# Kernel tuning notes

Measured on AMD Instinct MI355X. Metric: run time of the kernel, lower is better.

## Reference

```python
import jax, jax.numpy as jnp
import numpy as np

B, S, HID = 4, 4096, 1024
HEADS, D = 8, 128          # head_dim = HID // HEADS
NSEG, SEGLEN = 16, 256     # SEGLEN = S // NSEG
E, I = 16, 512             # num_experts, intermediate_size


def setup_inputs() -> dict:
    key = jax.random.key(0)
    ks = jax.random.split(key, 8)
    return {
        "x": jax.random.normal(ks[0], (B, S, HID), jnp.float32),
        "W_mh": jax.random.normal(ks[1], (HID, HID), jnp.float32) * (1.0 / np.sqrt(HID)),
        "b_mh": jax.random.normal(ks[2], (HID,), jnp.float32) * 0.02,
        "W_merge": jax.random.normal(ks[3], (HID, HID), jnp.float32) * (1.0 / np.sqrt(HID)),
        "b_merge": jnp.zeros((HID,), jnp.float32),
        "expert_embeddings": jax.random.normal(ks[4], (D, E), jnp.float32) * (1.0 / np.sqrt(D)),
        "first_linear": jax.random.normal(ks[5], (E, I, D), jnp.float32) * (1.0 / np.sqrt(D)),
        "second_linear": jax.random.normal(ks[6], (E, D, I), jnp.float32) * (1.0 / np.sqrt(I)),
    }


def reference(x, W_mh, b_mh, W_merge, b_merge, expert_embeddings, first_linear, second_linear):
    # multi-head projection
    x = x @ W_mh.T + b_mh                                   # [B,S,HID]
    # split into segments/heads (faithful to torch reshape order)
    x = x.reshape(B, NSEG, SEGLEN, HEADS, D)                # [B,N,L,H,D]
    avg = jnp.mean(x, axis=2)                               # [B,N,H,D]
    # router: softmax over experts
    ew = jax.nn.softmax(jnp.einsum('bnhd,de->bnhe', avg, expert_embeddings), axis=-1)
    # merge expert weight matrices (equivalent to torch's broadcast-mul-sum)
    m1 = jnp.einsum('eid,bnhe->bnhid', first_linear, ew)    # [B,N,H,I,D]
    m2 = jnp.einsum('edi,bnhe->bnhdi', second_linear, ew)   # [B,N,H,D,I]
    # NOTE: torch uses reshape (not permute) here -> mixes seglen/head axes; replicate.
    xr = x.reshape(B, NSEG, HEADS, SEGLEN, D)               # [B,N,H,L,D]
    # causal shift: segment s uses weights from segment s-1
    x_causal = xr[:, 1:]
    h = jax.nn.relu(jnp.einsum('bnhld,bnhid->bnhli', x_causal, m1[:, :-1]))
    res = jnp.einsum('bnhli,bnhdi->bnhld', h, m2[:, :-1])   # [B,N-1,H,L,D]
    # segment 0 special case (no_grad in torch -> stop_gradient)
    h0 = jax.nn.relu(jnp.einsum('bhld,bhid->bhli', xr[:, 0], m1[:, 0]))
    r0 = jnp.einsum('bhli,bhdi->bhld', h0, m2[:, 0])
    r0 = jax.lax.stop_gradient(r0)[:, None]                 # [B,1,H,L,D]
    out = jnp.concatenate([r0, res], axis=1)                # [B,N,H,L,D]
    out = out.reshape(B, S, HEADS, D).reshape(B, S, HID)
    return out @ W_merge.T + b_merge
```

## Files before the change

### kernel.cpp

```cpp
#include <hip/hip_runtime.h>
#include <hip/hip_bf16.h>

typedef _Float16 f16;
typedef f16 f16x2 __attribute__((ext_vector_type(2)));
typedef f16 f16x4 __attribute__((ext_vector_type(4)));
typedef f16 f16x8 __attribute__((ext_vector_type(8)));
typedef float f32x2 __attribute__((ext_vector_type(2)));
typedef float f32x4 __attribute__((ext_vector_type(4)));

#define MFMA16(a, b, c) __builtin_amdgcn_mfma_f32_16x16x32_f16(a, b, c, 0, 0, 0)

__device__ __forceinline__ void glds16(const void* g, void* l) {
    __builtin_amdgcn_global_load_lds(
        (const __attribute__((address_space(1))) unsigned int*)g,
        (__attribute__((address_space(3))) unsigned int*)l, 16, 0, 0);
}

__global__ __launch_bounds__(256) void cvt_kernel(const float* __restrict__ s,
                                                  f16* __restrict__ d, int n) {
    int i = (blockIdx.x * 256 + threadIdx.x) * 8;
    if (i >= n) return;
    float4 a = *(const float4*)(s + i);
    float4 b = *(const float4*)(s + i + 4);
    f16x8 h;
    h[0] = (f16)a.x; h[1] = (f16)a.y; h[2] = (f16)a.z; h[3] = (f16)a.w;
    h[4] = (f16)b.x; h[5] = (f16)b.y; h[6] = (f16)b.z; h[7] = (f16)b.w;
    *(f16x8*)(d + i) = h;
}

template <bool OUT_F16>
__global__ __launch_bounds__(256) void gemm_bt_kernel(
    const f16* __restrict__ A16, const f16* __restrict__ Bw,
    const float* __restrict__ bias, void* __restrict__ C_, int M, int N, int K) {
    __shared__ f16 As[128 * 32];
    __shared__ f16 Bs[128 * 32];
    const int tid = threadIdx.x;
    const int lane = tid & 63;
    const int w = tid >> 6;
    const int nblk = N >> 7;
    const int cpx = (int)gridDim.x >> 3;
    const int logical = ((int)blockIdx.x & 7) * cpx + ((int)blockIdx.x >> 3);
    const int mb = logical / nblk, nb = logical % nblk;
    const int wm = w >> 1, wn = w & 1;
    const int q = lane >> 4, cl = lane & 15;

    const f16* Bbase = Bw + (size_t)nb * 128 * K;

    f32x4 acc[4][4] = {};

#pragma unroll 1
    for (int kt = 0; kt < (K >> 5); ++kt) {
        const int k0 = kt << 5;
#pragma unroll
        for (int it = 0; it < 2; ++it) {
            int c = it * 256 + w * 64 + lane;
            glds16(Bbase + (size_t)(c >> 2) * K + k0 + (c & 3) * 8,
                   &Bs[(it * 256 + w * 64) * 8]);
        }
#pragma unroll
        for (int it = 0; it < 2; ++it) {
            int c = it * 256 + w * 64 + lane;
            glds16(A16 + (size_t)(mb * 128 + (c >> 2)) * K + k0 + (c & 3) * 8,
                   &As[(it * 256 + w * 64) * 8]);
        }
        __syncthreads();
        f16x8 af[4], bf[4];
#pragma unroll
        for (int mt = 0; mt < 4; ++mt)
            af[mt] = *(const f16x8*)&As[(wm * 64 + mt * 16 + cl) * 32 + q * 8];
#pragma unroll
        for (int nt = 0; nt < 4; ++nt)
            bf[nt] = *(const f16x8*)&Bs[(wn * 64 + nt * 16 + cl) * 32 + q * 8];
#pragma unroll
        for (int mt = 0; mt < 4; ++mt)
#pragma unroll
            for (int nt = 0; nt < 4; ++nt)
                acc[mt][nt] = MFMA16(af[mt], bf[nt], acc[mt][nt]);
        __syncthreads();
    }
    float bv[4];
#pragma unroll
    for (int nt = 0; nt < 4; ++nt) bv[nt] = bias[nb * 128 + wn * 64 + nt * 16 + cl];
#pragma unroll
    for (int mt = 0; mt < 4; ++mt) {
#pragma unroll
        for (int nt = 0; nt < 4; ++nt) {
            size_t gr = (size_t)(mb * 128 + wm * 64 + mt * 16 + q * 4);
            int gc = nb * 128 + wn * 64 + nt * 16 + cl;
#pragma unroll
            for (int r = 0; r < 4; ++r) {
                float v = acc[mt][nt][r] + bv[nt];
                if (OUT_F16)
                    ((f16*)C_)[(gr + r) * N + gc] = (f16)v;
                else
                    ((float*)C_)[(gr + r) * N + gc] = v;
            }
        }
    }
}

__global__ __launch_bounds__(256) void avg_kernel(const f16* __restrict__ X1h,
                                                  float* __restrict__ partial) {
    const int bn = blockIdx.x >> 2, rc = blockIdx.x & 3;
    const int tid = threadIdx.x;
    const f16* base = X1h + (size_t)bn * 262144 + (size_t)rc * 65536 + tid * 4;
    float s0 = 0.f, s1 = 0.f, s2 = 0.f, s3 = 0.f;
    for (int l = 0; l < 64; ++l) {
        f16x4 v = *(const f16x4*)(base + (size_t)l * 1024);
        s0 += (float)v[0]; s1 += (float)v[1]; s2 += (float)v[2]; s3 += (float)v[3];
    }
    const float sc = 1.f / 256.f;
    float4 o = make_float4(s0 * sc, s1 * sc, s2 * sc, s3 * sc);
    *(float4*)(partial + (size_t)(bn * 4 + rc) * 1024 + tid * 4) = o;
}

__global__ __launch_bounds__(64) void router_kernel(const float* __restrict__ partial,
                                                    const float* __restrict__ emb,
                                                    float* __restrict__ ew) {
    const int t = blockIdx.x;
    const int bn = t >> 3, h = t & 7;
    const int lane = threadIdx.x;
    float acc = 0.f;
    const float* p = partial + (size_t)bn * 4096 + h * 128;
    if (lane < 16) {
        for (int d = 0; d < 128; ++d) {
            float a = p[d] + p[d + 1024] + p[d + 2048] + p[d + 3072];
            acc = fmaf(a, emb[d * 16 + lane], acc);
        }
    }
    float m = acc;
#pragma unroll
    for (int o = 8; o; o >>= 1) m = fmaxf(m, __shfl_xor(m, o));
    float pr = __expf(acc - m);
    float s = pr;
#pragma unroll
    for (int o = 8; o; o >>= 1) s += __shfl_xor(s, o);
    if (lane < 16) ew[t * 16 + lane] = pr / s;
}

__global__ __launch_bounds__(256) void mix_kernel(const float* __restrict__ ew,
                                                  const float* __restrict__ FL,
                                                  const float* __restrict__ SL,
                                                  f16* __restrict__ m1h,
                                                  f16* __restrict__ m2h) {
    const int bid = blockIdx.x;
    const int which = bid >> 10;
    const int tg = (bid >> 6) & 15;
    const int chunk = bid & 63;
    const float* src = which ? SL : FL;
    f16* dst = which ? m2h : m1h;
    const int tid = threadIdx.x;
    const int e0 = chunk * 1024 + tid * 4;

    f32x4 fl[16];
#pragma unroll
    for (int e = 0; e < 16; ++e)
        fl[e] = *(const f32x4*)(src + (size_t)e * 65536 + e0);

    const float* wbase = ew + (size_t)tg * 32 * 16;
    float wc[16];
#pragma unroll
    for (int e = 0; e < 16; ++e) wc[e] = wbase[e];

#pragma unroll 1
    for (int tt = 0; tt < 32; ++tt) {
        float wn[16];
        if (tt < 31) {
#pragma unroll
            for (int e = 0; e < 16; ++e) wn[e] = wbase[(tt + 1) * 16 + e];
        }
        f32x4 a = {0.f, 0.f, 0.f, 0.f};
#pragma unroll
        for (int e = 0; e < 16; ++e) {
            a[0] = fmaf(wc[e], fl[e][0], a[0]);
            a[1] = fmaf(wc[e], fl[e][1], a[1]);
            a[2] = fmaf(wc[e], fl[e][2], a[2]);
            a[3] = fmaf(wc[e], fl[e][3], a[3]);
        }
        f16x4 h;
        h[0] = (f16)a[0]; h[1] = (f16)a[1]; h[2] = (f16)a[2]; h[3] = (f16)a[3];
        *(f16x4*)(dst + (size_t)(tg * 32 + tt) * 65536 + e0) = h;
        if (tt < 31) {
#pragma unroll
            for (int e = 0; e < 16; ++e) wc[e] = wn[e];
        }
    }
}

__device__ __forceinline__ void stage_w128(const f16* __restrict__ src, f16* lds,
                                           int w, int lane, int rowstride) {
#pragma unroll
    for (int it = 0; it < 8; ++it) {
        int cbase = it * 256 + w * 64;
        int c = cbase + lane;
        int row = c >> 4, pc = c & 15;
        int lc = pc ^ (row & 7);
        glds16(src + (size_t)row * rowstride + lc * 8, lds + cbase * 8);
    }
}

__global__ __launch_bounds__(256) void mlp_kernel(const f16* __restrict__ Xg,
                                                  const f16* __restrict__ m1h,
                                                  const f16* __restrict__ m2h,
                                                  f16* __restrict__ Yg) {
    __shared__ f16 Hs[128 * 128];
    __shared__ f16 Ws[128 * 128];
    const int cpx = (int)gridDim.x >> 3;
    const int logical = ((int)blockIdx.x & 7) * cpx + ((int)blockIdx.x >> 3);
    const int t = logical >> 1, lh = logical & 1;
    const int n = (t >> 3) & 15;
    const int tm = (n > 0) ? (t - 8) : t;
    const int tid = threadIdx.x;
    const int lane = tid & 63, w = tid >> 6;
    const int q = lane >> 4, cl = lane & 15;
    const int l0 = w * 32;

    const f16* Xsrc = Xg + (size_t)t * 32768 + lh * 16384;
    const f16* m1b = m1h + (size_t)tm * 65536;
    const f16* m2b = m2h + (size_t)tm * 65536;

    f16x8 xf[2][4];
#pragma unroll
    for (int lt = 0; lt < 2; ++lt) {
        int l = l0 + lt * 16 + cl;
#pragma unroll
        for (int ks = 0; ks < 4; ++ks)
            xf[lt][ks] = *(const f16x8*)(Xsrc + (size_t)l * 128 + ks * 32 + q * 8);
    }
    stage_w128(m1b, Ws, w, lane, 128);
    __syncthreads();

    f32x4 acc2[2][8] = {};
#pragma unroll 1
    for (int ic = 0; ic < 4; ++ic) {
#pragma unroll
        for (int it = 0; it < 8; ++it) {
            f16x8 af[4];
#pragma unroll
            for (int ks = 0; ks < 4; ++ks) {
                int r = it * 16 + cl;
                int ch = (ks * 4 + q) ^ (r & 7);
                af[ks] = *(const f16x8*)&Ws[r * 128 + ch * 8];
            }
            f32x4 a1[2] = {};
#pragma unroll
            for (int ks = 0; ks < 4; ++ks)
#pragma unroll
                for (int lt = 0; lt < 2; ++lt)
                    a1[lt] = MFMA16(af[ks], xf[lt][ks], a1[lt]);
            int ibase = it * 16 + q * 4;
            int ch = ibase >> 3;
            int sub = (q & 1) * 8;
#pragma unroll
            for (int lt = 0; lt < 2; ++lt) {
                int l = l0 + lt * 16 + cl;
                f16x4 hv;
                hv[0] = (f16)fmaxf(a1[lt][0], 0.f);
                hv[1] = (f16)fmaxf(a1[lt][1], 0.f);
                hv[2] = (f16)fmaxf(a1[lt][2], 0.f);
                hv[3] = (f16)fmaxf(a1[lt][3], 0.f);
                *(f16x4*)((char*)Hs + (size_t)l * 256 + ((ch ^ (l & 7)) << 4) + sub) = hv;
            }
        }
        __syncthreads();
        stage_w128(m2b + ic * 128, Ws, w, lane, 512);
        __syncthreads();

        f16x8 hf[2][4];
#pragma unroll
        for (int lt = 0; lt < 2; ++lt) {
            int l = l0 + lt * 16 + cl;
#pragma unroll
            for (int ks = 0; ks < 4; ++ks) {
                int ch = (ks * 4 + q) ^ (l & 7);
                hf[lt][ks] = *(const f16x8*)&Hs[l * 128 + ch * 8];
            }
        }
#pragma unroll
        for (int nt = 0; nt < 8; ++nt) {
            f16x8 bf[4];
#pragma unroll
            for (int ks = 0; ks < 4; ++ks) {
                int r = nt * 16 + cl;
                int ch = (ks * 4 + q) ^ (r & 7);
                bf[ks] = *(const f16x8*)&Ws[r * 128 + ch * 8];
            }
#pragma unroll
            for (int lt = 0; lt < 2; ++lt)
#pragma unroll
                for (int ks = 0; ks < 4; ++ks)
                    acc2[lt][nt] = MFMA16(hf[lt][ks], bf[ks], acc2[lt][nt]);
        }
        __syncthreads();
        if (ic < 3) {
            stage_w128(m1b + (size_t)(ic + 1) * 16384, Ws, w, lane, 128);
            __syncthreads();
        }
    }
    f16* Yb = Yg + (size_t)t * 32768 + lh * 16384;
#pragma unroll
    for (int lt = 0; lt < 2; ++lt) {
#pragma unroll
        for (int nt = 0; nt < 8; ++nt) {
            int lr = l0 + lt * 16 + q * 4;
            int d = nt * 16 + cl;
#pragma unroll
            for (int r = 0; r < 4; ++r)
                Yb[(size_t)(lr + r) * 128 + d] = (f16)acc2[lt][nt][r];
        }
    }
}

extern "C" void kernel_launch(void* const* d_in, const int* in_sizes, int n_in,
                              void* d_out, int out_size, void* d_ws, size_t ws_size,
                              hipStream_t stream) {
    const float* x    = (const float*)d_in[0];
    const float* W_mh = (const float*)d_in[1];
    const float* b_mh = (const float*)d_in[2];
    const float* W_mg = (const float*)d_in[3];
    const float* b_mg = (const float*)d_in[4];
    const float* emb  = (const float*)d_in[5];
    const float* FL   = (const float*)d_in[6];
    const float* SL   = (const float*)d_in[7];

    char* ws = (char*)d_ws;
    f16*   X1h  = (f16*)(ws + 0);
    f16*   m1h  = (f16*)(ws + 33554432);
    f16*   X0h  = (f16*)(ws + 33554432);
    f16*   m2h  = (f16*)(ws + 100663296);
    f16*   Wmhh = (f16*)(ws + 167772160);
    f16*   Wmgh = (f16*)(ws + 169869312);
    float* part = (float*)(ws + 171966464);
    float* ew   = (float*)(ws + 173015040);

    cvt_kernel<<<512, 256, 0, stream>>>(W_mh, Wmhh, 1048576);
    cvt_kernel<<<512, 256, 0, stream>>>(W_mg, Wmgh, 1048576);
    cvt_kernel<<<8192, 256, 0, stream>>>(x, X0h, 16777216);
    gemm_bt_kernel<true><<<1024, 256, 0, stream>>>(X0h, Wmhh, b_mh, X1h,
                                                   16384, 1024, 1024);
    avg_kernel<<<256, 256, 0, stream>>>(X1h, part);
    router_kernel<<<512, 64, 0, stream>>>(part, emb, ew);
    mix_kernel<<<2048, 256, 0, stream>>>(ew, FL, SL, m1h, m2h);
    mlp_kernel<<<1024, 256, 0, stream>>>(X1h, m1h, m2h, X1h);
    gemm_bt_kernel<false><<<1024, 256, 0, stream>>>(X1h, Wmgh, b_mg, d_out,
                                                    16384, 1024, 1024);
}
```

Baseline: 237.8 us.

## Replace projection GEMMs with 256x256 double-buffered, phase-pipelined MFMA kernel

Both dense projection GEMMs now run in a new kernel with 256x256 output tiles, 512 threads, and K-steps of 64. LDS tiles are split into halves and double-buffered, loaded asynchronously into LDS with an XOR swizzle, and scheduled as eight interleaved phases with explicit vmcnt waits, barriers and s_setprio around the MFMA blocks. The aim is to overlap global loads with matrix math and to cut LDS and global traffic per FLOP compared with the old 128x128 single-buffer kernel that synchronised on every K=32 step. In exchange it uses much more LDS and registers, launches only 256 blocks, and relies on hand-counted waitcnt values being correct.

After: 209.5 us. 11.9% less time.

```diff
diff --git a/kernel.cpp b/kernel.cpp
--- a/kernel.cpp
+++ b/kernel.cpp
@@ -28,72 +28,137 @@
     *(f16x8*)(d + i) = h;
 }
 
+
+template <int MH, int NH, bool LOADA>
+__device__ __forceinline__ void phase_rw(const f16* Aslab, const f16* Bslab,
+                                         f16x8 (&af)[4][2], f16x8 (&bf)[2][2],
+                                         int cl, int q, int wm, int wn) {
+    if (LOADA) {
+#pragma unroll
+        for (int mt = 0; mt < 4; ++mt)
+#pragma unroll
+            for (int ks = 0; ks < 2; ++ks)
+                af[mt][ks] =
+                    *(const f16x8*)&Aslab[(wm * 64 + mt * 16 + cl) * 64 +
+                                          ((ks * 4 + q) ^ (cl & 7)) * 8];
+    }
+#pragma unroll
+    for (int nt = 0; nt < 2; ++nt)
+#pragma unroll
+        for (int ks = 0; ks < 2; ++ks)
+            bf[nt][ks] = *(const f16x8*)&Bslab[(wn * 32 + nt * 16 + cl) * 64 +
+                                               ((ks * 4 + q) ^ (cl & 7)) * 8];
+}
+
+template <int MH, int NH>
+__device__ __forceinline__ void phase_mm(f16x8 (&af)[4][2], f16x8 (&bf)[2][2],
+                                         f32x4 (&acc)[8][4]) {
+    __builtin_amdgcn_s_setprio(1);
+#pragma unroll
+    for (int mt = 0; mt < 4; ++mt)
+#pragma unroll
+        for (int nt = 0; nt < 2; ++nt)
+#pragma unroll
+            for (int ks = 0; ks < 2; ++ks)
+                acc[MH * 4 + mt][NH * 2 + nt] =
+                    MFMA16(af[mt][ks], bf[nt][ks], acc[MH * 4 + mt][NH * 2 + nt]);
+    __builtin_amdgcn_s_setprio(0);
+}
+
+__device__ __forceinline__ void stage_half(const f16* gsrc, int ldk, f16* ldst,
+                                           int w, int lane) {
+#pragma unroll
+    for (int j = 0; j < 2; ++j) {
+        int idx = j * 512 + w * 64 + lane;
+        int rr = idx >> 3;
+        int gs = (idx & 7) ^ (rr & 7);
+        glds16(gsrc + (size_t)rr * ldk + gs * 8, ldst + (j * 512 + w * 64) * 8);
+    }
+}
+
+#define VM8 asm volatile("s_waitcnt vmcnt(8)" ::: "memory")
+#define VM6 asm volatile("s_waitcnt vmcnt(6)" ::: "memory")
+#define VM4 asm volatile("s_waitcnt vmcnt(4)" ::: "memory")
+#define VM0 asm volatile("s_waitcnt vmcnt(0)" ::: "memory")
+#define VMN do {} while (0)
+#define SB0 __builtin_amdgcn_sched_barrier(0)
+
+#define SA(DB, H, KT) stage_half(A16 + (size_t)(mb * 256 + (H)*128) * K + (KT)*64, \
+                                 K, Ad[DB][H], w, lane)
+#define SBm(DB, H, KT) stage_half(Bw + (size_t)(nb * 256 + (H)*128) * K + (KT)*64, \
+                                  K, Bd[DB][H], w, lane)
+
+#define PH(DB, MH, NH, LA, STAGE, VMC)                                    \
+    phase_rw<MH, NH, LA>(Ad[DB][MH], Bd[DB][NH], af, bf, cl, q, wm, wn);  \
+    STAGE;                                                                \
+    SB0; __builtin_amdgcn_s_barrier(); SB0;                               \
+    phase_mm<MH, NH>(af, bf, acc);                                        \
+    VMC;                                                                  \
+    SB0; __builtin_amdgcn_s_barrier(); SB0;
+
 template <bool OUT_F16>
-__global__ __launch_bounds__(256) void gemm_bt_kernel(
+__global__ __launch_bounds__(512, 2) void gemm256_kernel(
     const f16* __restrict__ A16, const f16* __restrict__ Bw,
     const float* __restrict__ bias, void* __restrict__ C_, int M, int N, int K) {
-    __shared__ f16 As[128 * 32];
-    __shared__ f16 Bs[128 * 32];
+    __shared__ f16 Ad[2][2][128 * 64];
+    __shared__ f16 Bd[2][2][128 * 64];
     const int tid = threadIdx.x;
     const int lane = tid & 63;
     const int w = tid >> 6;
-    const int nblk = N >> 7;
+    const int wm = w >> 2, wn = w & 3;
+    const int q = lane >> 4, cl = lane & 15;
+    const int nblk = N >> 8;
     const int cpx = (int)gridDim.x >> 3;
     const int logical = ((int)blockIdx.x & 7) * cpx + ((int)blockIdx.x >> 3);
     const int mb = logical / nblk, nb = logical % nblk;
-    const int wm = w >> 1, wn = w & 1;
-    const int q = lane >> 4, cl = lane & 15;
-
-    const f16* Bbase = Bw + (size_t)nb * 128 * K;
-
-    f32x4 acc[4][4] = {};
+
+    f32x4 acc[8][4] = {};
+    f16x8 af[4][2], bf[2][2];
+    const int ITERS = (K >> 6) / 2;
+
+    SA(0, 0, 0); SBm(0, 0, 0); SBm(0, 1, 0); SA(0, 1, 0);
+    SA(1, 0, 1); SBm(1, 0, 1);
+    VM8;
+    SB0; __builtin_amdgcn_s_barrier(); SB0;
 
 #pragma unroll 1
-    for (int kt = 0; kt < (K >> 5); ++kt) {
-        const int k0 = kt << 5;
-#pragma unroll
-        for (int it = 0; it < 2; ++it) {
-            int c = it * 256 + w * 64 + lane;
-            glds16(Bbase + (size_t)(c >> 2) * K + k0 + (c & 3) * 8,
-                   &Bs[(it * 256 + w * 64) * 8]);
-        }
-#pragma unroll
-        for (int it = 0; it < 2; ++it) {
-            int c = it * 256 + w * 64 + lane;
-            glds16(A16 + (size_t)(mb * 128 + (c >> 2)) * K + k0 + (c & 3) * 8,
-                   &As[(it * 256 + w * 64) * 8]);
-        }
-        __syncthreads();
-        f16x8 af[4], bf[4];
-#pragma unroll
-        for (int mt = 0; mt < 4; ++mt)
-            af[mt] = *(const f16x8*)&As[(wm * 64 + mt * 16 + cl) * 32 + q * 8];
-#pragma unroll
-        for (int nt = 0; nt < 4; ++nt)
-            bf[nt] = *(const f16x8*)&Bs[(wn * 64 + nt * 16 + cl) * 32 + q * 8];
-#pragma unroll
-        for (int mt = 0; mt < 4; ++mt)
-#pragma unroll
-            for (int nt = 0; nt < 4; ++nt)
-                acc[mt][nt] = MFMA16(af[mt], bf[nt], acc[mt][nt]);
-        __syncthreads();
-    }
-    float bv[4];
-#pragma unroll
-    for (int nt = 0; nt < 4; ++nt) bv[nt] = bias[nb * 128 + wn * 64 + nt * 16 + cl];
-#pragma unroll
-    for (int mt = 0; mt < 4; ++mt) {
-#pragma unroll
-        for (int nt = 0; nt < 4; ++nt) {
-            size_t gr = (size_t)(mb * 128 + wm * 64 + mt * 16 + q * 4);
-            int gc = nb * 128 + wn * 64 + nt * 16 + cl;
+    for (int i = 0; i < ITERS - 1; ++i) {
+        const int k2 = 2 * i;
+        PH(0, 0, 0, true,  SA(1, 1, k2 + 1),  VM8)
+        PH(0, 0, 1, false, SBm(1, 1, k2 + 1), VM8)
+        PH(0, 1, 0, true,  SA(0, 0, k2 + 2),  VMN)
+        PH(0, 1, 1, false, SBm(0, 0, k2 + 2), VM8)
+        PH(1, 0, 0, true,  SBm(0, 1, k2 + 2), VM6)
+        PH(1, 0, 1, false, SA(0, 1, k2 + 2),  VMN)
+        PH(1, 1, 0, true,  SA(1, 0, k2 + 3),  VMN)
+        PH(1, 1, 1, false, SBm(1, 0, k2 + 3), VM8)
+    }
+    {
+        const int kl = 2 * ITERS - 1;
+        PH(0, 0, 0, true,  SA(1, 1, kl),  VM8)
+        PH(0, 0, 1, false, SBm(1, 1, kl), VM8)
+        PH(0, 1, 0, true,  VMN,           VMN)
+        PH(0, 1, 1, false, VMN,           VM4)
+        PH(1, 0, 0, true,  VMN,           VM0)
+        PH(1, 0, 1, false, VMN,           VMN)
+        PH(1, 1, 0, true,  VMN,           VMN)
+        PH(1, 1, 1, false, VMN,           VMN)
+    }
+
+#pragma unroll
+    for (int mt7 = 0; mt7 < 8; ++mt7) {
+#pragma unroll
+        for (int nt4 = 0; nt4 < 4; ++nt4) {
+            int row0 = mb * 256 + (mt7 >> 2) * 128 + wm * 64 + (mt7 & 3) * 16 + q * 4;
+            int col = nb * 256 + (nt4 >> 1) * 128 + wn * 32 + (nt4 & 1) * 16 + cl;
+            float bv = bias[col];
 #pragma unroll
             for (int r = 0; r < 4; ++r) {
-                float v = acc[mt][nt][r] + bv[nt];
+                float v = acc[mt7][nt4][r] + bv;
                 if (OUT_F16)
-                    ((f16*)C_)[(gr + r) * N + gc] = (f16)v;
+                    ((f16*)C_)[(size_t)(row0 + r) * N + col] = (f16)v;
                 else
-                    ((float*)C_)[(gr + r) * N + gc] = v;
+                    ((float*)C_)[(size_t)(row0 + r) * N + col] = v;
             }
         }
     }
@@ -164,10 +229,10 @@
 
 #pragma unroll 1
     for (int tt = 0; tt < 32; ++tt) {
-        float wn[16];
+        float wn2[16];
         if (tt < 31) {
 #pragma unroll
-            for (int e = 0; e < 16; ++e) wn[e] = wbase[(tt + 1) * 16 + e];
+            for (int e = 0; e < 16; ++e) wn2[e] = wbase[(tt + 1) * 16 + e];
         }
         f32x4 a = {0.f, 0.f, 0.f, 0.f};
 #pragma unroll
@@ -182,7 +247,7 @@
         *(f16x4*)(dst + (size_t)(tg * 32 + tt) * 65536 + e0) = h;
         if (tt < 31) {
 #pragma unroll
-            for (int e = 0; e < 16; ++e) wc[e] = wn[e];
+            for (int e = 0; e < 16; ++e) wc[e] = wn2[e];
         }
     }
 }
@@ -235,19 +300,19 @@
     for (int ic = 0; ic < 4; ++ic) {
 #pragma unroll
         for (int it = 0; it < 8; ++it) {
-            f16x8 af[4];
+            f16x8 af2[4];
 #pragma unroll
             for (int ks = 0; ks < 4; ++ks) {
                 int r = it * 16 + cl;
                 int ch = (ks * 4 + q) ^ (r & 7);
-                af[ks] = *(const f16x8*)&Ws[r * 128 + ch * 8];
+                af2[ks] = *(const f16x8*)&Ws[r * 128 + ch * 8];
             }
             f32x4 a1[2] = {};
 #pragma unroll
             for (int ks = 0; ks < 4; ++ks)
 #pragma unroll
                 for (int lt = 0; lt < 2; ++lt)
-                    a1[lt] = MFMA16(af[ks], xf[lt][ks], a1[lt]);
+                    a1[lt] = MFMA16(af2[ks], xf[lt][ks], a1[lt]);
             int ibase = it * 16 + q * 4;
             int ch = ibase >> 3;
             int sub = (q & 1) * 8;
@@ -278,18 +343,18 @@
         }
 #pragma unroll
         for (int nt = 0; nt < 8; ++nt) {
-            f16x8 bf[4];
+            f16x8 bf2[4];
 #pragma unroll
             for (int ks = 0; ks < 4; ++ks) {
                 int r = nt * 16 + cl;
                 int ch = (ks * 4 + q) ^ (r & 7);
-                bf[ks] = *(const f16x8*)&Ws[r * 128 + ch * 8];
+                bf2[ks] = *(const f16x8*)&Ws[r * 128 + ch * 8];
             }
 #pragma unroll
             for (int lt = 0; lt < 2; ++lt)
 #pragma unroll
                 for (int ks = 0; ks < 4; ++ks)
-                    acc2[lt][nt] = MFMA16(hf[lt][ks], bf[ks], acc2[lt][nt]);
+                    acc2[lt][nt] = MFMA16(hf[lt][ks], bf2[ks], acc2[lt][nt]);
         }
         __syncthreads();
         if (ic < 3) {
@@ -336,12 +401,12 @@
     cvt_kernel<<<512, 256, 0, stream>>>(W_mh, Wmhh, 1048576);
     cvt_kernel<<<512, 256, 0, stream>>>(W_mg, Wmgh, 1048576);
     cvt_kernel<<<8192, 256, 0, stream>>>(x, X0h, 16777216);
-    gemm_bt_kernel<true><<<1024, 256, 0, stream>>>(X0h, Wmhh, b_mh, X1h,
-                                                   16384, 1024, 1024);
+    gemm256_kernel<true><<<256, 512, 0, stream>>>(X0h, Wmhh, b_mh, X1h,
+                                                  16384, 1024, 1024);
     avg_kernel<<<256, 256, 0, stream>>>(X1h, part);
     router_kernel<<<512, 64, 0, stream>>>(part, emb, ew);
     mix_kernel<<<2048, 256, 0, stream>>>(ew, FL, SL, m1h, m2h);
     mlp_kernel<<<1024, 256, 0, stream>>>(X1h, m1h, m2h, X1h);
-    gemm_bt_kernel<false><<<1024, 256, 0, stream>>>(X1h, Wmgh, b_mg, d_out,
-                                                    16384, 1024, 1024);
-}
+    gemm256_kernel<false><<<256, 512, 0, stream>>>(X1h, Wmgh, b_mg, d_out,
+                                                   16384, 1024, 1024);
+}
```
